# Performance work log

Hardware: AMD Instinct MI355X
Metric: run time of the kernel (lower is better)

The kernel has to match this reference:

```python
import jax, jax.numpy as jnp
import numpy as np
from jax import lax

P = 8; E = 192; D_MODEL = E + 4; D_STATE = 16; D_CONV = 4; EXPAND = 2
D_INNER = EXPAND * D_MODEL  # 392
DT_RANK = -(-D_MODEL // 16)  # 13
MAX_FREQ = 32


def silu(v):
    return v * jax.nn.sigmoid(v)


def layernorm(v, g, b, eps=1e-5):
    m = v.mean(-1, keepdims=True)
    var = v.var(-1, keepdims=True)
    return (v - m) / jnp.sqrt(var + eps) * g + b


def mamba(x, in_w, conv_w, conv_b, xp_w, dt_w, dt_b, A_log, Dp, out_w):
    # Standard mamba_ssm Mamba block. x: (B, L, d_model)
    B, L, _ = x.shape
    xz = x @ in_w.T                      # (B,L,2*d_inner)
    xi, z = jnp.split(xz, 2, axis=-1)
    # depthwise causal conv1d (torch pads d_conv-1 both sides then truncates to L)
    xc = jnp.transpose(xi, (0, 2, 1))    # (B,d_inner,L)
    xc = lax.conv_general_dilated(xc, conv_w[:, None, :], (1,), [(D_CONV - 1, 0)],
                                  dimension_numbers=('NCH', 'OIH', 'NCH'),
                                  feature_group_count=D_INNER)
    xc = silu(jnp.transpose(xc, (0, 2, 1)) + conv_b)  # (B,L,d_inner)
    x_dbl = xc @ xp_w.T                  # (B,L,dt_rank+2*d_state)
    dt = x_dbl[..., :DT_RANK]
    Bm = x_dbl[..., DT_RANK:DT_RANK + D_STATE]
    Cm = x_dbl[..., DT_RANK + D_STATE:]
    delta = jax.nn.softplus(dt @ dt_w.T + dt_b)       # (B,L,d_inner)
    A = -jnp.exp(A_log)                               # (d_inner,d_state)
    deltaA = jnp.exp(delta[..., None] * A)            # (B,L,d_inner,d_state)
    deltaBu = delta[..., None] * Bm[:, :, None, :] * xc[..., None]

    def step(h, inp):
        dA, dBu, c = inp
        h = dA * h + dBu
        return h, jnp.einsum('bdn,bn->bd', h, c)

    h0 = jnp.zeros((B, D_INNER, D_STATE), x.dtype)
    _, ys = lax.scan(step, h0, (deltaA.transpose(1, 0, 2, 3),
                                deltaBu.transpose(1, 0, 2, 3),
                                Cm.transpose(1, 0, 2)))
    y = ys.transpose(1, 0, 2) + Dp * xc
    y = y * silu(z)
    return y @ out_w.T


def _mk_mamba_params(key):
    ks = jax.random.split(key, 6)
    s = 0.05
    return dict(
        in_w=jax.random.normal(ks[0], (2 * D_INNER, D_MODEL)) * s,
        conv_w=jax.random.normal(ks[1], (D_INNER, D_CONV)) * s,
        conv_b=jnp.zeros((D_INNER,)),
        xp_w=jax.random.normal(ks[2], (DT_RANK + 2 * D_STATE, D_INNER)) * s,
        dt_w=jax.random.normal(ks[3], (D_INNER, DT_RANK)) * s,
        dt_b=jax.random.normal(ks[4], (D_INNER,)) * 0.1,
        A_log=jnp.log(jnp.broadcast_to(jnp.arange(1, D_STATE + 1, dtype=jnp.float32), (D_INNER, D_STATE)) + 0.0),
        D=jnp.ones((D_INNER,)),
        out_w=jax.random.normal(ks[5], (D_MODEL, D_INNER)) * s,
    )


def setup_inputs() -> dict:
    key = jax.random.key(0)
    k = jax.random.split(key, 8)
    inp = {
        'x': jax.random.normal(k[0], (16, 3, 256, 256), dtype=jnp.float32),
        'patch_w': jax.random.normal(k[1], (E, 3, P, P)) * 0.05,
        'patch_b': jnp.zeros((E,)),
        'pe_ln_g': jnp.ones((E,)), 'pe_ln_b': jnp.zeros((E,)),
        'blk_ln_g': jnp.ones((D_MODEL,)), 'blk_ln_b': jnp.zeros((D_MODEL,)),
        'cls_w': jax.random.normal(k[2], (1, D_MODEL)) * 0.05,
        'cls_b': jnp.zeros((1,)),
    }
    for pref, kk in (('f_', k[3]), ('b_', k[4])):
        for name, val in _mk_mamba_params(kk).items():
            inp[pref + name] = val
    return inp


def reference(x, patch_w, patch_b, pe_ln_g, pe_ln_b,
              f_in_w, f_conv_w, f_conv_b, f_xp_w, f_dt_w, f_dt_b, f_A_log, f_D, f_out_w,
              b_in_w, b_conv_w, b_conv_b, b_xp_w, b_dt_w, b_dt_b, b_A_log, b_D, b_out_w,
              blk_ln_g, blk_ln_b, cls_w, cls_b):
    B, C, H, W = x.shape
    hp, wp = H // P, W // P
    # PatchEmbed: stride==kernel conv expressed as one GEMM over patches
    xp = x.reshape(B, C, hp, P, wp, P)
    tok = jnp.einsum('bchpwq,ecpq->bhwe', xp, patch_w) + patch_b
    tok = tok.reshape(B, hp * wp, E)
    tok = silu(layernorm(tok, pe_ln_g, pe_ln_b))
    # RotaryEmbedding: concat 4 positional channels
    L = hp * wp
    scale = 2 * np.pi / MAX_FREQ
    pos = jnp.arange(L, dtype=tok.dtype)[:, None] * scale
    row = (jnp.arange(L) // MAX_FREQ).astype(tok.dtype)[:, None] * scale
    cp = jnp.concatenate([jnp.sin(pos), jnp.cos(pos), jnp.sin(row), jnp.cos(row)], axis=-1)
    h = jnp.concatenate([tok, jnp.broadcast_to(cp[None], (B, L, 4))], axis=-1)  # (B,L,196)
    # BidirectionalMambaBlock
    fo = mamba(h, f_in_w, f_conv_w, f_conv_b, f_xp_w, f_dt_w, f_dt_b, f_A_log, f_D, f_out_w)
    bo = jnp.flip(mamba(jnp.flip(h, 1), b_in_w, b_conv_w, b_conv_b, b_xp_w, b_dt_w, b_dt_b, b_A_log, b_D, b_out_w), 1)
    out = (fo + bo) * 0.5
    out = silu(layernorm(out, blk_ln_g, blk_ln_b)) + h
    # Classifier: mean pool + linear (num_classes==2 -> 1 logit)
    return out.mean(1) @ cls_w.T + cls_b
```

## Files before the change

### kernel.cpp

```cpp
#include <hip/hip_runtime.h>
#include <cstdint>
#include <cstddef>

constexpr int B_   = 16;
constexpr int L_   = 1024;
constexpr int E_   = 192;
constexpr int DM   = 196;
constexpr int DI   = 392;
constexpr int DS   = 16;
constexpr int DTR  = 13;
constexpr int NTOK = B_ * L_;
constexpr int XDW  = DTR + 2 * DS;
constexpr int CH   = B_ * DI;

constexpr int KP_XZ = 224;
constexpr int KP_OP = 416;
constexpr int KP_PW = 192;

constexpr size_t HW_SZ = (size_t)NTOK * DM;
constexpr size_t DI_SZ = (size_t)NTOK * DI;

constexpr size_t O_H     = 0;
constexpr size_t O_H16   = 3211264;
constexpr size_t O_XI_F  = 5046272;
constexpr size_t O_XI_B  = 11468800;
constexpr size_t O_Z_F   = 17891328;
constexpr size_t O_Z_B   = 24313856;
constexpr size_t O_XC_F  = 30736384;
constexpr size_t O_XC_B  = 37158912;
constexpr size_t O_DTR_F = 43581440;
constexpr size_t O_DTR_B = 43794432;
constexpr size_t O_BC_F  = 44007424;
constexpr size_t O_BC_B  = 44531712;
constexpr size_t O_YS_F  = 45056000;
constexpr size_t O_YS_B  = 48267264;
constexpr size_t O_PW16  = 51478528;
constexpr size_t O_FIN16 = 51496960;
constexpr size_t O_BIN16 = 51584768;
constexpr size_t O_FOUT16= 51672576;
constexpr size_t O_BOUT16= 51713344;

typedef _Float16 half8 __attribute__((ext_vector_type(8)));
typedef _Float16 half4v __attribute__((ext_vector_type(4)));
typedef float f32x4v __attribute__((ext_vector_type(4)));

__device__ __forceinline__ float siluf(float x) {
    return x / (1.f + __expf(-x));
}
__device__ __forceinline__ float fexp2(float x) {
    return __builtin_amdgcn_exp2f(x);
}

__device__ __forceinline__ float blk_sum(float v, float* red) {
    #pragma unroll
    for (int o = 32; o > 0; o >>= 1) v += __shfl_down(v, o);
    int w = threadIdx.x >> 6;
    __syncthreads();
    if ((threadIdx.x & 63) == 0) red[w] = v;
    __syncthreads();
    return red[0] + red[1] + red[2] + red[3];
}

__global__ __launch_bounds__(256) void cvt_all(const float* __restrict__ pw,
                                               const float* __restrict__ fin,
                                               const float* __restrict__ bin,
                                               const float* __restrict__ fout,
                                               const float* __restrict__ bout,
                                               _Float16* __restrict__ dst) {
    int i = blockIdx.x * 256 + threadIdx.x;
    const float* src; int K, Kp, off;
    if (i < 36864)       { src = pw;   K = 192; Kp = 192; off = i; }
    else if (i < 212480) { src = fin;  K = 196; Kp = 224; off = i - 36864; }
    else if (i < 388096) { src = bin;  K = 196; Kp = 224; off = i - 212480; }
    else if (i < 469632) { src = fout; K = 392; Kp = 416; off = i - 388096; }
    else                 { src = bout; K = 392; Kp = 416; off = i - 469632; }
    int n = off / Kp, k = off - n * Kp;
    dst[i] = (_Float16)(k < K ? src[(size_t)n * K + k] : 0.f);
}

__global__ __launch_bounds__(256) void gather_patch(const float* __restrict__ x,
                                                    _Float16* __restrict__ Xp) {
    int i = blockIdx.x * 256 + threadIdx.x;
    int tok = i / 24, r = i - tok * 24;
    int c = r >> 3, p = r & 7;
    int b = tok >> 10, l = tok & 1023, hh = l >> 5, wv = l & 31;
    const float* src = x + (((size_t)(b * 3 + c) * 256 + hh * 8 + p) << 8) + wv * 8;
    float4 v0 = *(const float4*)src;
    float4 v1 = *(const float4*)(src + 4);
    half8 o;
    o[0] = (_Float16)v0.x; o[1] = (_Float16)v0.y; o[2] = (_Float16)v0.z; o[3] = (_Float16)v0.w;
    o[4] = (_Float16)v1.x; o[5] = (_Float16)v1.y; o[6] = (_Float16)v1.z; o[7] = (_Float16)v1.w;
    *(half8*)(Xp + (size_t)tok * 192 + c * 64 + p * 8) = o;
}

template <int MODE>
__device__ __forceinline__ void mfma_core(const _Float16* __restrict__ A,
                                          const _Float16* __restrict__ W,
                                          const float* __restrict__ bias,
                                          void* __restrict__ Cv_,
                                          int N, int Kpad, int ldc,
                                          int flip, int m_blk, int n_blk) {
    const int tid = threadIdx.x;
    const int wv = tid >> 6, lane = tid & 63;
    const int col = lane & 15, quad = lane >> 4;
    const int m_base = m_blk * 128 + wv * 32;
    const int n_base = n_blk * 64;

    int r0 = m_base + col, r1 = m_base + 16 + col;
    if (flip) {
        r0 = (r0 & ~1023) + (1023 - (r0 & 1023));
        r1 = (r1 & ~1023) + (1023 - (r1 & 1023));
    }
    const _Float16* a0p = A + (size_t)r0 * Kpad + quad * 8;
    const _Float16* a1p = A + (size_t)r1 * Kpad + quad * 8;

    const _Float16* bp[4];
    bool bok[4];
    #pragma unroll
    for (int j = 0; j < 4; ++j) {
        int n = n_base + j * 16 + col;
        bok[j] = (n < N);
        bp[j] = W + (size_t)(bok[j] ? n : 0) * Kpad + quad * 8;
    }

    f32x4v acc[2][4];
    #pragma unroll
    for (int i = 0; i < 2; ++i)
        #pragma unroll
        for (int j = 0; j < 4; ++j)
            #pragma unroll
            for (int r = 0; r < 4; ++r) acc[i][j][r] = 0.f;

    half8 bzero;
    #pragma unroll
    for (int q = 0; q < 8; ++q) bzero[q] = (_Float16)0.f;

    for (int k0 = 0; k0 < Kpad; k0 += 32) {
        half8 a0 = *(const half8*)(a0p + k0);
        half8 a1 = *(const half8*)(a1p + k0);
        #pragma unroll
        for (int j = 0; j < 4; ++j) {
            half8 bv = bzero;
            if (bok[j]) bv = *(const half8*)(bp[j] + k0);
            acc[0][j] = __builtin_amdgcn_mfma_f32_16x16x32_f16(a0, bv, acc[0][j], 0, 0, 0);
            acc[1][j] = __builtin_amdgcn_mfma_f32_16x16x32_f16(a1, bv, acc[1][j], 0, 0, 0);
        }
    }

    if constexpr (MODE == 0) {
        float* C = (float*)Cv_;
        #pragma unroll
        for (int i = 0; i < 2; ++i) {
            int mrow = m_base + i * 16 + quad * 4;
            #pragma unroll
            for (int j = 0; j < 4; ++j) {
                int n = n_base + j * 16 + col;
                if (n < N) {
                    float bv = bias ? bias[n] : 0.f;
                    #pragma unroll
                    for (int r = 0; r < 4; ++r)
                        C[(size_t)(mrow + r) * ldc + n] = acc[i][j][r] + bv;
                }
            }
        }
    } else if constexpr (MODE == 2 || MODE == 3) {
        __shared__ _Float16 cst[64 * 136];
        #pragma unroll
        for (int i = 0; i < 2; ++i) {
            int t_loc = wv * 32 + i * 16 + quad * 4;
            #pragma unroll
            for (int j = 0; j < 4; ++j) {
                int n_loc = j * 16 + col;
                half4v v;
                #pragma unroll
                for (int r = 0; r < 4; ++r) {
                    float xx = acc[i][j][r];
                    if (MODE == 3) xx = xx / (1.f + __expf(-xx));
                    v[r] = (_Float16)xx;
                }
                *(half4v*)&cst[n_loc * 136 + t_loc] = v;
            }
        }
        __syncthreads();
        const int n_loc = tid >> 2, chunk = tid & 3;
        const int n = n_base + n_loc;
        if (n < N) {
            const int bb = (m_blk * 128) >> 10;
            const int t0b = (m_blk * 128) & 1023;
            _Float16* dst = (_Float16*)Cv_ + (((size_t)(bb * N + n)) << 10) + t0b + chunk * 32;
            const _Float16* s = &cst[n_loc * 136 + chunk * 32];
            #pragma unroll
            for (int q = 0; q < 4; ++q)
                *(half8*)(dst + q * 8) = *(const half8*)(s + q * 8);
        }
    } else {
        __shared__ _Float16 cst[128 * 72];
        #pragma unroll
        for (int i = 0; i < 2; ++i) {
            #pragma unroll
            for (int j = 0; j < 4; ++j) {
                int n_loc = j * 16 + col;
                #pragma unroll
                for (int r = 0; r < 4; ++r) {
                    int m_loc = wv * 32 + i * 16 + quad * 4 + r;
                    cst[m_loc * 72 + n_loc] = (_Float16)acc[i][j][r];
                }
            }
        }
        __syncthreads();
        const int m_loc = tid >> 1, half = tid & 1;
        const int m = m_blk * 128 + m_loc;
        _Float16* C = (_Float16*)Cv_;
        const _Float16* s = &cst[m_loc * 72 + half * 32];
        if (n_base + 64 <= N) {
            _Float16* dst = C + (size_t)m * ldc + n_base + half * 32;
            #pragma unroll
            for (int q = 0; q < 4; ++q)
                *(half8*)(dst + q * 8) = *(const half8*)(s + q * 8);
        } else {
            #pragma unroll
            for (int q = 0; q < 32; ++q) {
                int n = n_base + half * 32 + q;
                if (n < N) C[(size_t)m * ldc + n] = s[q];
            }
        }
    }
}

__global__ __launch_bounds__(256) void mfma_patch(const _Float16* __restrict__ A,
                                                  const _Float16* __restrict__ W,
                                                  const float* __restrict__ bias,
                                                  float* __restrict__ C) {
    mfma_core<0>(A, W, bias, C, 192, KP_PW, 192, 0, blockIdx.x, blockIdx.y);
}

__global__ __launch_bounds__(256) void mfma_xz(const _Float16* __restrict__ A,
                                               const _Float16* __restrict__ Wf,
                                               const _Float16* __restrict__ Wb,
                                               _Float16* __restrict__ C0, _Float16* __restrict__ C1,
                                               _Float16* __restrict__ C2, _Float16* __restrict__ C3) {
    const int zi = blockIdx.z;
    const _Float16* W = (zi < 2 ? Wf : Wb) + (size_t)(zi & 1) * DI * KP_XZ;
    const int flip = zi >> 1;
    if (zi == 0)      mfma_core<2>(A, W, nullptr, C0, DI, KP_XZ, 0, flip, blockIdx.x, blockIdx.y);
    else if (zi == 1) mfma_core<3>(A, W, nullptr, C1, DI, KP_XZ, 0, flip, blockIdx.x, blockIdx.y);
    else if (zi == 2) mfma_core<2>(A, W, nullptr, C2, DI, KP_XZ, 0, flip, blockIdx.x, blockIdx.y);
    else              mfma_core<3>(A, W, nullptr, C3, DI, KP_XZ, 0, flip, blockIdx.x, blockIdx.y);
}

__global__ __launch_bounds__(256) void mfma_op(const _Float16* __restrict__ Af,
                                               const _Float16* __restrict__ Ab,
                                               const _Float16* __restrict__ Wf,
                                               const _Float16* __restrict__ Wb,
                                               _Float16* __restrict__ Cf, _Float16* __restrict__ Cb) {
    const int zi = blockIdx.z;
    mfma_core<4>(zi ? Ab : Af, zi ? Wb : Wf, nullptr, zi ? Cb : Cf,
                 DM, KP_OP, DM, 0, blockIdx.x, blockIdx.y);
}

__global__ __launch_bounds__(256) void ln_silu_pos(const float* __restrict__ tok,
                                                   const float* __restrict__ g,
                                                   const float* __restrict__ bb,
                                                   _Float16* __restrict__ h16) {
    const int w = threadIdx.x >> 6, lane = threadIdx.x & 63;
    const int t = blockIdx.x * 4 + w;
    const float* tp = tok + (size_t)t * E_;
    float v[3];
    float s1 = 0.f, s2 = 0.f;
    #pragma unroll
    for (int i = 0; i < 3; ++i) {
        v[i] = tp[lane + i * 64];
        s1 += v[i];
        s2 = fmaf(v[i], v[i], s2);
    }
    #pragma unroll
    for (int o = 32; o > 0; o >>= 1) {
        s1 += __shfl_xor(s1, o);
        s2 += __shfl_xor(s2, o);
    }
    float mean = s1 * (1.f / E_);
    float var = s2 * (1.f / E_) - mean * mean;
    float inv = rsqrtf(var + 1e-5f);
    _Float16* hq = h16 + (size_t)t * KP_XZ;
    #pragma unroll
    for (int i = 0; i < 3; ++i) {
        int e = lane + i * 64;
        float o = siluf((v[i] - mean) * inv * g[e] + bb[e]);
        hq[e] = (_Float16)o;
    }
    const int l = t & 1023;
    const float scale = 0.19634954084936207f;
    if (lane < 4) {
        float pv = (lane == 0) ? sinf(l * scale)
                 : (lane == 1) ? cosf(l * scale)
                 : (lane == 2) ? sinf((float)(l >> 5) * scale)
                 :               cosf((float)(l >> 5) * scale);
        hq[E_ + lane] = (_Float16)pv;
    } else if (lane < 32) {
        hq[192 + lane] = (_Float16)0.f;
    }
}

__global__ __launch_bounds__(256) void gemm_xdbl(const _Float16* __restrict__ xi_f,
                                                 const _Float16* __restrict__ xi_b,
                                                 const float* __restrict__ Wf,
                                                 const float* __restrict__ Wb,
                                                 const float* __restrict__ fcw,
                                                 const float* __restrict__ fcb,
                                                 const float* __restrict__ bcw,
                                                 const float* __restrict__ bcb,
                                                 float* __restrict__ dtrf,
                                                 float* __restrict__ dtrb,
                                                 float* __restrict__ bcf,
                                                 float* __restrict__ bcb2,
                                                 _Float16* __restrict__ xcf,
                                                 _Float16* __restrict__ xcb) {
    const int yi = blockIdx.y;
    const _Float16* xi = yi ? xi_b : xi_f;
    const float* W = yi ? Wb : Wf;
    const float* cw = yi ? bcw : fcw;
    const float* cb = yi ? bcb : fcb;
    float* dtr = yi ? dtrb : dtrf;
    float* bc = yi ? bcb2 : bcf;
    _Float16* xc = yi ? xcb : xcf;
    __shared__ __align__(16) float As[16][68];
    __shared__ __align__(16) float Ws[16][68];
    const int m0 = blockIdx.x * 64;
    const int t = threadIdx.x;
    const int tx = t & 15, ty = t >> 4;
    float acc[4][4] = {};
    const int arow_l = t >> 2;
    const int kq = (t & 3) * 4;
    const int bb_ = m0 >> 10, tt0 = m0 & 1023;
    for (int kt = 0; kt < 25; ++kt) {
        const int k0 = kt << 4;
        {
            int kr = t >> 4, tc = t & 15;
            int kk = k0 + kr;
            float o4[4] = {0.f, 0.f, 0.f, 0.f};
            if (kk < DI) {
                const int tpos = tt0 + tc * 4;
                const _Float16* xp = xi + (((size_t)(bb_ * DI + kk)) << 10) + tpos;
                half4v cur = *(const half4v*)xp;
                half4v prv;
                if (tpos > 0) prv = *(const half4v*)(xp - 4);
                else { prv[0] = prv[1] = prv[2] = prv[3] = (_Float16)0.f; }
                float xw[7] = {(float)prv[1], (float)prv[2], (float)prv[3],
                               (float)cur[0], (float)cur[1], (float)cur[2], (float)cur[3]};
                float4 wv4 = *(const float4*)(cw + kk * 4);
                float wc[4] = {wv4.x, wv4.y, wv4.z, wv4.w};
                float bv = cb[kk];
                #pragma unroll
                for (int j = 0; j < 4; ++j) {
                    float a = bv;
                    #pragma unroll
                    for (int q = 0; q < 4; ++q) a = fmaf(xw[j + q], wc[q], a);
                    o4[j] = siluf(a);
                }
                half4v o4h;
                #pragma unroll
                for (int j = 0; j < 4; ++j) o4h[j] = (_Float16)o4[j];
                *(half4v*)(xc + (((size_t)(bb_ * DI + kk)) << 10) + tpos) = o4h;
            }
            *(float4*)&As[kr][tc * 4] = *(float4*)o4;
        }
        {
            bool okn = arow_l < XDW;
            const float* wp = W + (size_t)arow_l * DI;
            #pragma unroll
            for (int jj = 0; jj < 4; ++jj) {
                int kk = k0 + kq + jj;
                Ws[kq + jj][arow_l] = (okn && kk < DI) ? wp[kk] : 0.f;
            }
        }
        __syncthreads();
        #pragma unroll
        for (int k = 0; k < 16; ++k) {
            float av[4], wv[4];
            *(float4*)av = *(const float4*)&As[k][ty * 4];
            *(float4*)wv = *(const float4*)&Ws[k][tx * 4];
            #pragma unroll
            for (int i = 0; i < 4; ++i)
                #pragma unroll
                for (int j = 0; j < 4; ++j)
                    acc[i][j] = fmaf(av[i], wv[j], acc[i][j]);
        }
        __syncthreads();
    }
    #pragma unroll
    for (int i = 0; i < 4; ++i) {
        int m = m0 + ty * 4 + i;
        #pragma unroll
        for (int j = 0; j < 4; ++j) {
            int n = tx * 4 + j;
            float v = acc[i][j];
            if (n < DTR) dtr[(size_t)m * DTR + n] = v;
            else if (n < XDW) bc[(size_t)m * 32 + (n - DTR)] = v;
        }
    }
}

__global__ __launch_bounds__(256) void delta_kernel(
        const float* __restrict__ dtr_f, const float* __restrict__ dtr_b,
        _Float16* __restrict__ dlT_f, _Float16* __restrict__ dlT_b,
        const float* __restrict__ f_dt_w, const float* __restrict__ f_dt_b,
        const float* __restrict__ b_dt_w, const float* __restrict__ b_dt_b) {
    int i = blockIdx.x * 256 + threadIdx.x;
    int dir = i >= (int)DI_SZ;
    int j = dir ? i - (int)DI_SZ : i;
    int r = j >> 10, t = j & 1023;
    int b = r / DI, d = r - (r / DI) * DI;
    size_t tok = ((size_t)b << 10) + t;
    const float* xd = (dir ? dtr_b : dtr_f) + tok * DTR;
    const float* w = (dir ? b_dt_w : f_dt_w) + d * DTR;
    float acc = (dir ? b_dt_b : f_dt_b)[d];
    #pragma unroll
    for (int q = 0; q < DTR; ++q) acc = fmaf(xd[q], w[q], acc);
    float sp = fmaxf(acc, 0.f) + log1pf(__expf(-fabsf(acc)));
    (dir ? dlT_b : dlT_f)[j] = (_Float16)sp;
}

__global__ __launch_bounds__(256) void scan_kernel(
        const _Float16* __restrict__ dlT_f, const _Float16* __restrict__ dlT_b,
        const _Float16* __restrict__ xcT_f, const _Float16* __restrict__ xcT_b,
        const float* __restrict__ bc_f,  const float* __restrict__ bc_b,
        const _Float16* __restrict__ zT_f, const _Float16* __restrict__ zT_b,
        _Float16* __restrict__ y16_f,    _Float16* __restrict__ y16_b,
        const float* __restrict__ fA, const float* __restrict__ bA,
        const float* __restrict__ fD, const float* __restrict__ bD) {
    __shared__ float sP[8][8][16];
    __shared__ float sH[8][8][16];
    __shared__ float sI[8][8][16];
    const int tid = threadIdx.x;
    const int ni = tid & 3;
    const int c  = (tid >> 2) & 7;
    const int ch_l = tid >> 5;
    const int chain = blockIdx.x * 8 + ch_l;
    const int dir = chain >= CH;
    const int r = chain - (dir ? CH : 0);
    const int b = r / DI, d = r - (r / DI) * DI;

    const _Float16* dlT = (dir ? dlT_b : dlT_f) + ((size_t)r << 10);
    const _Float16* uT  = (dir ? xcT_b : xcT_f) + ((size_t)r << 10);
    const _Float16* zT = (dir ? zT_b : zT_f) + ((size_t)r << 10);
    const float* BC  = (dir ? bc_b  : bc_f)  + (((size_t)b << 10) * 32);
    _Float16* y16    = (dir ? y16_b : y16_f) + ((size_t)r << 10);
    const float* Al  = (dir ? bA : fA) + d * DS + ni * 4;
    float Av[4];
    #pragma unroll
    for (int i = 0; i < 4; ++i) Av[i] = -__expf(Al[i]) * 1.4426950408889634f;
    const float Dd = (dir ? bD : fD)[d];
    const int t0 = c << 7;

    if (c < 7) {
        float h[4] = {0.f, 0.f, 0.f, 0.f};
        float S = 0.f;
        const float* bcp = BC + t0 * 32 + ni * 4;
        const _Float16* dp = dlT + t0;
        const _Float16* up = uT + t0;
        for (int g = 0; g < 32; ++g) {
            half4v d4 = *(const half4v*)(dp + g * 4);
            half4v u4 = *(const half4v*)(up + g * 4);
            float dv[4] = {(float)d4[0], (float)d4[1], (float)d4[2], (float)d4[3]};
            float uv[4] = {(float)u4[0], (float)u4[1], (float)u4[2], (float)u4[3]};
            #pragma unroll
            for (int tt = 0; tt < 4; ++tt) {
                float4 B4 = *(const float4*)(bcp + tt * 32);
                float w = dv[tt] * uv[tt];
                S += dv[tt];
                float Bv[4] = {B4.x, B4.y, B4.z, B4.w};
                #pragma unroll
                for (int i = 0; i < 4; ++i)
                    h[i] = fmaf(fexp2(dv[tt] * Av[i]), h[i], w * Bv[i]);
            }
            bcp += 128;
        }
        #pragma unroll
        for (int i = 0; i < 4; ++i) {
            sP[ch_l][c][ni * 4 + i] = fexp2(S * Av[i]);
            sH[ch_l][c][ni * 4 + i] = h[i];
        }
    }
    __syncthreads();

    if (tid < 128) {
        const int ch = tid >> 4, n = tid & 15;
        float hi = 0.f;
        #pragma unroll
        for (int cc = 0; cc < 8; ++cc) {
            sI[ch][cc][n] = hi;
            if (cc < 7) hi = sH[ch][cc][n] + sP[ch][cc][n] * hi;
        }
    }
    __syncthreads();

    {
        float h[4];
        #pragma unroll
        for (int i = 0; i < 4; ++i) h[i] = sI[ch_l][c][ni * 4 + i];
        _Float16 ybuf[8] __attribute__((aligned(16)));
        half8 zb;
        const float* bcp = BC + t0 * 32 + ni * 4;
        const _Float16* dp = dlT + t0;
        const _Float16* up = uT + t0;
        for (int g = 0; g < 32; ++g) {
            if ((g & 7) == 0)
                zb = *(const half8*)(zT + t0 + ((g >> 3) << 5) + ni * 8);
            half4v d4 = *(const half4v*)(dp + g * 4);
            half4v u4 = *(const half4v*)(up + g * 4);
            float dv[4] = {(float)d4[0], (float)d4[1], (float)d4[2], (float)d4[3]};
            float uv[4] = {(float)u4[0], (float)u4[1], (float)u4[2], (float)u4[3]};
            float pq[4];
            #pragma unroll
            for (int tt = 0; tt < 4; ++tt) {
                float4 B4 = *(const float4*)(bcp + tt * 32);
                float4 C4 = *(const float4*)(bcp + tt * 32 + 16);
                float w = dv[tt] * uv[tt];
                float Bv[4] = {B4.x, B4.y, B4.z, B4.w};
                float Cv[4] = {C4.x, C4.y, C4.z, C4.w};
                float p = 0.f;
                #pragma unroll
                for (int i = 0; i < 4; ++i) {
                    h[i] = fmaf(fexp2(dv[tt] * Av[i]), h[i], w * Bv[i]);
                    p = fmaf(h[i], Cv[i], p);
                }
                pq[tt] = p;
            }
            bcp += 128;
            #pragma unroll
            for (int tt = 0; tt < 4; ++tt) {
                pq[tt] += __shfl_xor(pq[tt], 1);
                pq[tt] += __shfl_xor(pq[tt], 2);
            }
            if (((g >> 1) & 3) == ni) {
                const int base = (g & 1) * 4;
                #pragma unroll
                for (int tt = 0; tt < 4; ++tt)
                    ybuf[base + tt] =
                        (_Float16)((pq[tt] + Dd * uv[tt]) * (float)zb[base + tt]);
            }
            if ((g & 7) == 7)
                *(half8*)(y16 + t0 + ((g >> 3) << 5) + ni * 8) = *(half8*)ybuf;
        }
    }
}

__global__ __launch_bounds__(256) void transp_y(
        const _Float16* __restrict__ yf, const _Float16* __restrict__ yb,
        _Float16* __restrict__ of, _Float16* __restrict__ ob) {
    __shared__ _Float16 tile[64][72];
    const int dblk = blockIdx.z % 7, dir = blockIdx.z / 7;
    const int b = blockIdx.y, tb = blockIdx.x;
    const _Float16* y = dir ? yb : yf;
    _Float16* o = dir ? ob : of;
    const int d0 = dblk * 64, t0 = tb * 64;
    const int dl = threadIdx.x >> 2, ts = (threadIdx.x & 3) * 16;
    const int d = d0 + dl;
    if (d < DI) {
        const _Float16* src = y + (((size_t)(b * DI + d)) << 10) + t0 + ts;
        *(half8*)&tile[dl][ts] = *(const half8*)src;
        *(half8*)&tile[dl][ts + 8] = *(const half8*)(src + 8);
    } else {
        #pragma unroll
        for (int q = 0; q < 16; ++q) tile[dl][ts + q] = (_Float16)0.f;
    }
    __syncthreads();
    const int tl = threadIdx.x >> 2, ds = (threadIdx.x & 3) * 16;
    if (d0 + ds < KP_OP) {
        _Float16 v[16] __attribute__((aligned(16)));
        #pragma unroll
        for (int q = 0; q < 16; ++q) v[q] = tile[ds + q][tl];
        _Float16* dst = o + ((size_t)((b << 10) + t0 + tl)) * KP_OP + d0 + ds;
        *(half8*)dst = *(half8*)&v[0];
        *(half8*)(dst + 8) = *(half8*)&v[8];
    }
}

__global__ __launch_bounds__(256) void final_head(
        const _Float16* __restrict__ fo, const _Float16* __restrict__ bo,
        const _Float16* __restrict__ h16, const float* __restrict__ g,
        const float* __restrict__ bb, const float* __restrict__ cls_w,
        float* __restrict__ partial) {
    const int w = threadIdx.x >> 6, lane = threadIdx.x & 63;
    const int t = blockIdx.x * 4 + w;
    const int b = t >> 10, l = t & 1023;
    const _Float16* fp = fo + (size_t)t * DM;
    const _Float16* bp = bo + ((size_t)(b << 10) + (1023 - l)) * DM;
    const _Float16* hp = h16 + (size_t)t * KP_XZ;
    float v[4];
    float s1 = 0.f, s2 = 0.f;
    #pragma unroll
    for (int i = 0; i < 4; ++i) {
        int e = lane + i * 64;
        bool ok = (i < 3) || (lane < 4);
        float vv = ok ? 0.5f * ((float)fp[e] + (float)bp[e]) : 0.f;
        v[i] = vv;
        s1 += vv;
        s2 = fmaf(vv, vv, s2);
    }
    #pragma unroll
    for (int o = 32; o > 0; o >>= 1) {
        s1 += __shfl_xor(s1, o);
        s2 += __shfl_xor(s2, o);
    }
    float mean = s1 * (1.f / DM);
    float var = s2 * (1.f / DM) - mean * mean;
    float inv = rsqrtf(var + 1e-5f);
    float c = 0.f;
    #pragma unroll
    for (int i = 0; i < 4; ++i) {
        int e = lane + i * 64;
        bool ok = (i < 3) || (lane < 4);
        if (ok) {
            float o2 = (v[i] - mean) * inv * g[e] + bb[e];
            o2 = siluf(o2) + (float)hp[e];
            c = fmaf(o2, cls_w[e], c);
        }
    }
    #pragma unroll
    for (int o = 32; o > 0; o >>= 1) c += __shfl_xor(c, o);
    if (lane == 0) partial[t] = c;
}

__global__ __launch_bounds__(256) void head_reduce(const float* __restrict__ partial,
                                                   const float* __restrict__ cls_b,
                                                   float* __restrict__ out) {
    __shared__ float red[4];
    const int b = blockIdx.x;
    const float* p = partial + ((size_t)b << 10);
    float s = 0.f;
    for (int i = threadIdx.x; i < 1024; i += 256) s += p[i];
    s = blk_sum(s, red);
    if (threadIdx.x == 0) out[b] = s * (1.f / 1024.f) + cls_b[0];
}

extern "C" void kernel_launch(void* const* d_in, const int* in_sizes, int n_in,
                              void* d_out, int out_size, void* d_ws, size_t ws_size,
                              hipStream_t stream) {
    const float* x        = (const float*)d_in[0];
    const float* patch_w  = (const float*)d_in[1];
    const float* patch_b  = (const float*)d_in[2];
    const float* pe_g     = (const float*)d_in[3];
    const float* pe_b     = (const float*)d_in[4];
    const float* blk_g    = (const float*)d_in[5];
    const float* blk_b    = (const float*)d_in[6];
    const float* cls_w    = (const float*)d_in[7];
    const float* cls_b    = (const float*)d_in[8];
    const float* f_in_w   = (const float*)d_in[9];
    const float* f_conv_w = (const float*)d_in[10];
    const float* f_conv_b = (const float*)d_in[11];
    const float* f_xp_w   = (const float*)d_in[12];
    const float* f_dt_w   = (const float*)d_in[13];
    const float* f_dt_b   = (const float*)d_in[14];
    const float* f_A_log  = (const float*)d_in[15];
    const float* f_D      = (const float*)d_in[16];
    const float* f_out_w  = (const float*)d_in[17];
    const float* b_in_w   = (const float*)d_in[18];
    const float* b_conv_w = (const float*)d_in[19];
    const float* b_conv_b = (const float*)d_in[20];
    const float* b_xp_w   = (const float*)d_in[21];
    const float* b_dt_w   = (const float*)d_in[22];
    const float* b_dt_b   = (const float*)d_in[23];
    const float* b_A_log  = (const float*)d_in[24];
    const float* b_D      = (const float*)d_in[25];
    const float* b_out_w  = (const float*)d_in[26];

    float* ws = (float*)d_ws;
    float* out = (float*)d_out;

    _Float16* H16    = (_Float16*)(ws + O_H16);
    _Float16* XI16f  = (_Float16*)(ws + O_XI_F);
    _Float16* XI16b  = (_Float16*)(ws + O_XI_B);
    _Float16* DL16f  = (_Float16*)(ws + O_XI_F);
    _Float16* DL16b  = (_Float16*)(ws + O_XI_B);
    _Float16* FO16   = (_Float16*)(ws + O_XI_F);
    _Float16* BO16   = (_Float16*)(ws + O_XI_B);
    _Float16* ZT16f  = (_Float16*)(ws + O_Z_F);
    _Float16* ZT16b  = (_Float16*)(ws + O_Z_B);
    _Float16* YsTf16 = (_Float16*)(ws + O_Z_F);
    _Float16* YsTb16 = (_Float16*)(ws + O_Z_B);
    _Float16* XC16f  = (_Float16*)(ws + O_XC_F);
    _Float16* XC16b  = (_Float16*)(ws + O_XC_B);
    float* PART      = ws + O_XC_F;
    float* DTRf      = ws + O_DTR_F;
    float* DTRb      = ws + O_DTR_B;
    float* BCf       = ws + O_BC_F;
    float* BCb       = ws + O_BC_B;
    _Float16* Xp16   = (_Float16*)(ws + O_YS_F);
    float* TokRaw    = ws + O_YS_B;
    _Float16* Y16f   = (_Float16*)(ws + O_YS_F);
    _Float16* Y16b   = (_Float16*)(ws + O_YS_B);
    _Float16* PW16   = (_Float16*)(ws + O_PW16);
    _Float16* FIN16  = (_Float16*)(ws + O_FIN16);
    _Float16* BIN16  = (_Float16*)(ws + O_BIN16);
    _Float16* FOUT16 = (_Float16*)(ws + O_FOUT16);
    _Float16* BOUT16 = (_Float16*)(ws + O_BOUT16);

    cvt_all<<<2153, 256, 0, stream>>>(patch_w, f_in_w, b_in_w, f_out_w, b_out_w, PW16);

    gather_patch<<<(NTOK * 24) / 256, 256, 0, stream>>>(x, Xp16);
    mfma_patch<<<dim3(NTOK / 128, 3), 256, 0, stream>>>(Xp16, PW16, patch_b, TokRaw);
    ln_silu_pos<<<NTOK / 4, 256, 0, stream>>>(TokRaw, pe_g, pe_b, H16);

    mfma_xz<<<dim3(NTOK / 128, 7, 4), 256, 0, stream>>>(H16, FIN16, BIN16,
                                                        XI16f, ZT16f, XI16b, ZT16b);
    gemm_xdbl<<<dim3(NTOK / 64, 2), 256, 0, stream>>>(
        XI16f, XI16b, f_xp_w, b_xp_w, f_conv_w, f_conv_b, b_conv_w, b_conv_b,
        DTRf, DTRb, BCf, BCb, XC16f, XC16b);
    delta_kernel<<<(2 * (int)DI_SZ) / 256, 256, 0, stream>>>(
        DTRf, DTRb, DL16f, DL16b, f_dt_w, f_dt_b, b_dt_w, b_dt_b);
    scan_kernel<<<2 * CH / 8, 256, 0, stream>>>(
        DL16f, DL16b, XC16f, XC16b, BCf, BCb, ZT16f, ZT16b, Y16f, Y16b,
        f_A_log, b_A_log, f_D, b_D);
    transp_y<<<dim3(16, 16, 14), 256, 0, stream>>>(Y16f, Y16b, YsTf16, YsTb16);
    mfma_op<<<dim3(NTOK / 128, 4, 2), 256, 0, stream>>>(YsTf16, YsTb16,
                                                        FOUT16, BOUT16, FO16, BO16);
    final_head<<<NTOK / 4, 256, 0, stream>>>(FO16, BO16, H16, blk_g, blk_b, cls_w, PART);
    head_reduce<<<B_, 256, 0, stream>>>(PART, cls_b, out);
}
```

Measured before the change: 474.1 us.

## Remap scan threads to 32 time-chunks with all 16 states per thread

The chunked selective scan now gives each thread all 16 state elements over a 32-step chunk, with 32 chunks per chain, instead of 4 states over a 128-step chunk across 8 chunks. This drops the cross-lane shuffles for the C·h reduction and shortens each thread's sequential chain. The cost is a longer 32-step serial prefix pass across chunks and more registers per thread, for which launch_bounds with 4 waves is added. Shared memory is padded to 17 columns to avoid bank conflicts, and two buffers replace three.

```diff
diff --git a/kernel.cpp b/kernel.cpp
--- a/kernel.cpp
+++ b/kernel.cpp
@@ -420,7 +420,7 @@
     (dir ? dlT_b : dlT_f)[j] = (_Float16)sp;
 }
 
-__global__ __launch_bounds__(256) void scan_kernel(
+__global__ __launch_bounds__(256, 4) void scan_kernel(
         const _Float16* __restrict__ dlT_f, const _Float16* __restrict__ dlT_b,
         const _Float16* __restrict__ xcT_f, const _Float16* __restrict__ xcT_b,
         const float* __restrict__ bc_f,  const float* __restrict__ bc_b,
@@ -428,13 +428,12 @@
         _Float16* __restrict__ y16_f,    _Float16* __restrict__ y16_b,
         const float* __restrict__ fA, const float* __restrict__ bA,
         const float* __restrict__ fD, const float* __restrict__ bD) {
-    __shared__ float sP[8][8][16];
-    __shared__ float sH[8][8][16];
-    __shared__ float sI[8][8][16];
+    __shared__ float sH[256][17];
+    __shared__ float sPI[256][17];
     const int tid = threadIdx.x;
-    const int ni = tid & 3;
-    const int c  = (tid >> 2) & 7;
-    const int ch_l = tid >> 5;
+    const int ch_l = tid & 7;
+    const int c    = tid >> 3;
+    const int row  = (c << 3) | ch_l;
     const int chain = blockIdx.x * 8 + ch_l;
     const int dir = chain >= CH;
     const int r = chain - (dir ? CH : 0);
@@ -442,43 +441,49 @@
 
     const _Float16* dlT = (dir ? dlT_b : dlT_f) + ((size_t)r << 10);
     const _Float16* uT  = (dir ? xcT_b : xcT_f) + ((size_t)r << 10);
-    const _Float16* zT = (dir ? zT_b : zT_f) + ((size_t)r << 10);
+    const _Float16* zT  = (dir ? zT_b : zT_f) + ((size_t)r << 10);
     const float* BC  = (dir ? bc_b  : bc_f)  + (((size_t)b << 10) * 32);
     _Float16* y16    = (dir ? y16_b : y16_f) + ((size_t)r << 10);
-    const float* Al  = (dir ? bA : fA) + d * DS + ni * 4;
-    float Av[4];
-    #pragma unroll
-    for (int i = 0; i < 4; ++i) Av[i] = -__expf(Al[i]) * 1.4426950408889634f;
+    const float* Al  = (dir ? bA : fA) + d * DS;
+    float Av[16];
+    #pragma unroll
+    for (int i = 0; i < 16; ++i) Av[i] = -__expf(Al[i]) * 1.4426950408889634f;
     const float Dd = (dir ? bD : fD)[d];
-    const int t0 = c << 7;
-
-    if (c < 7) {
-        float h[4] = {0.f, 0.f, 0.f, 0.f};
+    const int t0 = c << 5;
+
+    if (c < 31) {
+        float h[16];
+        #pragma unroll
+        for (int i = 0; i < 16; ++i) h[i] = 0.f;
         float S = 0.f;
-        const float* bcp = BC + t0 * 32 + ni * 4;
+        const float* bcp = BC + t0 * 32;
         const _Float16* dp = dlT + t0;
         const _Float16* up = uT + t0;
-        for (int g = 0; g < 32; ++g) {
+        for (int g = 0; g < 8; ++g) {
             half4v d4 = *(const half4v*)(dp + g * 4);
             half4v u4 = *(const half4v*)(up + g * 4);
-            float dv[4] = {(float)d4[0], (float)d4[1], (float)d4[2], (float)d4[3]};
-            float uv[4] = {(float)u4[0], (float)u4[1], (float)u4[2], (float)u4[3]};
             #pragma unroll
             for (int tt = 0; tt < 4; ++tt) {
-                float4 B4 = *(const float4*)(bcp + tt * 32);
-                float w = dv[tt] * uv[tt];
-                S += dv[tt];
-                float Bv[4] = {B4.x, B4.y, B4.z, B4.w};
+                float dv = (float)d4[tt];
+                float uv = (float)u4[tt];
+                float w = dv * uv;
+                S += dv;
+                float4 B0 = *(const float4*)(bcp + tt * 32);
+                float4 B1 = *(const float4*)(bcp + tt * 32 + 4);
+                float4 B2 = *(const float4*)(bcp + tt * 32 + 8);
+                float4 B3 = *(const float4*)(bcp + tt * 32 + 12);
+                float Bv[16] = {B0.x, B0.y, B0.z, B0.w, B1.x, B1.y, B1.z, B1.w,
+                                B2.x, B2.y, B2.z, B2.w, B3.x, B3.y, B3.z, B3.w};
                 #pragma unroll
-                for (int i = 0; i < 4; ++i)
-                    h[i] = fmaf(fexp2(dv[tt] * Av[i]), h[i], w * Bv[i]);
+                for (int i = 0; i < 16; ++i)
+                    h[i] = fmaf(fexp2(dv * Av[i]), h[i], w * Bv[i]);
             }
             bcp += 128;
         }
         #pragma unroll
-        for (int i = 0; i < 4; ++i) {
-            sP[ch_l][c][ni * 4 + i] = fexp2(S * Av[i]);
-            sH[ch_l][c][ni * 4 + i] = h[i];
+        for (int i = 0; i < 16; ++i) {
+            sPI[row][i] = fexp2(S * Av[i]);
+            sH[row][i] = h[i];
         }
     }
     __syncthreads();
@@ -487,60 +492,61 @@
         const int ch = tid >> 4, n = tid & 15;
         float hi = 0.f;
         #pragma unroll
-        for (int cc = 0; cc < 8; ++cc) {
-            sI[ch][cc][n] = hi;
-            if (cc < 7) hi = sH[ch][cc][n] + sP[ch][cc][n] * hi;
+        for (int cc = 0; cc < 32; ++cc) {
+            const int rw = (cc << 3) | ch;
+            float P = sPI[rw][n];
+            float H = sH[rw][n];
+            sPI[rw][n] = hi;
+            if (cc < 31) hi = fmaf(P, hi, H);
         }
     }
     __syncthreads();
 
     {
-        float h[4];
-        #pragma unroll
-        for (int i = 0; i < 4; ++i) h[i] = sI[ch_l][c][ni * 4 + i];
-        _Float16 ybuf[8] __attribute__((aligned(16)));
-        half8 zb;
-        const float* bcp = BC + t0 * 32 + ni * 4;
+        float h[16];
+        #pragma unroll
+        for (int i = 0; i < 16; ++i) h[i] = sPI[row][i];
+        const float* bcp = BC + t0 * 32;
         const _Float16* dp = dlT + t0;
         const _Float16* up = uT + t0;
-        for (int g = 0; g < 32; ++g) {
-            if ((g & 7) == 0)
-                zb = *(const half8*)(zT + t0 + ((g >> 3) << 5) + ni * 8);
-            half4v d4 = *(const half4v*)(dp + g * 4);
-            half4v u4 = *(const half4v*)(up + g * 4);
-            float dv[4] = {(float)d4[0], (float)d4[1], (float)d4[2], (float)d4[3]};
-            float uv[4] = {(float)u4[0], (float)u4[1], (float)u4[2], (float)u4[3]};
-            float pq[4];
-            #pragma unroll
-            for (int tt = 0; tt < 4; ++tt) {
-                float4 B4 = *(const float4*)(bcp + tt * 32);
-                float4 C4 = *(const float4*)(bcp + tt * 32 + 16);
-                float w = dv[tt] * uv[tt];
-                float Bv[4] = {B4.x, B4.y, B4.z, B4.w};
-                float Cv[4] = {C4.x, C4.y, C4.z, C4.w};
-                float p = 0.f;
+        const _Float16* zp = zT + t0;
+        _Float16* yp = y16 + t0;
+        for (int g8 = 0; g8 < 4; ++g8) {
+            half8 zb = *(const half8*)(zp + g8 * 8);
+            _Float16 ybuf[8] __attribute__((aligned(16)));
+            #pragma unroll
+            for (int gg = 0; gg < 2; ++gg) {
+                half4v d4 = *(const half4v*)(dp + g8 * 8 + gg * 4);
+                half4v u4 = *(const half4v*)(up + g8 * 8 + gg * 4);
                 #pragma unroll
-                for (int i = 0; i < 4; ++i) {
-                    h[i] = fmaf(fexp2(dv[tt] * Av[i]), h[i], w * Bv[i]);
-                    p = fmaf(h[i], Cv[i], p);
+                for (int tt = 0; tt < 4; ++tt) {
+                    float dv = (float)d4[tt];
+                    float uv = (float)u4[tt];
+                    float w = dv * uv;
+                    float4 B0 = *(const float4*)(bcp + tt * 32);
+                    float4 B1 = *(const float4*)(bcp + tt * 32 + 4);
+                    float4 B2 = *(const float4*)(bcp + tt * 32 + 8);
+                    float4 B3 = *(const float4*)(bcp + tt * 32 + 12);
+                    float4 C0 = *(const float4*)(bcp + tt * 32 + 16);
+                    float4 C1 = *(const float4*)(bcp + tt * 32 + 20);
+                    float4 C2 = *(const float4*)(bcp + tt * 32 + 24);
+                    float4 C3 = *(const float4*)(bcp + tt * 32 + 28);
+                    float Bv[16] = {B0.x, B0.y, B0.z, B0.w, B1.x, B1.y, B1.z, B1.w,
+                                    B2.x, B2.y, B2.z, B2.w, B3.x, B3.y, B3.z, B3.w};
+                    float Cv[16] = {C0.x, C0.y, C0.z, C0.w, C1.x, C1.y, C1.z, C1.w,
+                                    C2.x, C2.y, C2.z, C2.w, C3.x, C3.y, C3.z, C3.w};
+                    float p = 0.f;
+                    #pragma unroll
+                    for (int i = 0; i < 16; ++i) {
+                        h[i] = fmaf(fexp2(dv * Av[i]), h[i], w * Bv[i]);
+                        p = fmaf(h[i], Cv[i], p);
+                    }
+                    ybuf[gg * 4 + tt] =
+                        (_Float16)((p + Dd * uv) * (float)zb[gg * 4 + tt]);
                 }
-                pq[tt] = p;
+                bcp += 128;
             }
-            bcp += 128;
-            #pragma unroll
-            for (int tt = 0; tt < 4; ++tt) {
-                pq[tt] += __shfl_xor(pq[tt], 1);
-                pq[tt] += __shfl_xor(pq[tt], 2);
-            }
-            if (((g >> 1) & 3) == ni) {
-                const int base = (g & 1) * 4;
-                #pragma unroll
-                for (int tt = 0; tt < 4; ++tt)
-                    ybuf[base + tt] =
-                        (_Float16)((pq[tt] + Dd * uv[tt]) * (float)zb[base + tt]);
-            }
-            if ((g & 7) == 7)
-                *(half8*)(y16 + t0 + ((g >> 3) << 5) + ni * 8) = *(half8*)ybuf;
+            *(half8*)(yp + g8 * 8) = *(half8*)ybuf;
         }
     }
 }
```

New measurement: 522.6 us. 10.2% more time.
